# Kernel tuning notes

Measured on AMD Instinct MI355X. Metric: run time of the kernel, lower is better.

Reference implementation:

```python
import jax, jax.numpy as jnp
import numpy as np
from math import factorial, sqrt

# ---- configuration (matches init_kwargs) ----
MUL = 64
N = 32768
IRREPS1 = [(MUL, l) for l in range(3)]   # 64x0e + 64x1o + 64x2e
IRREPS2 = [(1, l) for l in range(3)]     # 1x0e + 1x1o + 1x2e (spherical harmonics)
IRREPS_OUT = [(MUL, l) for l in range(3)]
# (i_in1, i_in2, i_out) -- all parity/triangle-allowed uvw paths with l<=2
PATHS = [(0,0,0),(0,1,1),(0,2,2),(1,0,1),(1,1,0),(1,1,2),(1,2,1),(2,0,2),(2,1,1),(2,2,0),(2,2,2)]

# ---- real Clebsch-Gordan (e3nn convention: real basis, unit Frobenius norm) ----
def _su2_cg(j1, m1, j2, m2, j3, m3):
    if m3 != m1 + m2:
        return 0.0
    f = factorial
    vmin = max(-j1 + j2 + m3, -j1 + m1, 0)
    vmax = min(j2 + j3 + m1, j3 - j1 + j2, j3 + m3)
    C = sqrt((2*j3+1) * f(j3+j1-j2) * f(j3-j1+j2) * f(j1+j2-j3) * f(j3+m3) * f(j3-m3)
             / (f(j1+j2+j3+1) * f(j1-m1) * f(j1+m1) * f(j2-m2) * f(j2+m2)))
    S = 0.0
    for v in range(vmin, vmax + 1):
        S += (-1.0)**(v + j2 + m2) * f(j2+j3+m1-v) * f(j1-m1+v) / (f(v) * f(j3-j1+j2-v) * f(j3+m3-v) * f(v+j1-j2-m3))
    return C * S

def _su2_clebsch_gordan(j1, j2, j3):
    mat = np.zeros((2*j1+1, 2*j2+1, 2*j3+1))
    for m1 in range(-j1, j1+1):
        for m2 in range(-j2, j2+1):
            if abs(m1 + m2) <= j3:
                mat[j1+m1, j2+m2, j3+m1+m2] = _su2_cg(j1, m1, j2, m2, j3, m1+m2)
    return mat

def _change_basis_real_to_complex(l):
    q = np.zeros((2*l+1, 2*l+1), dtype=np.complex128)
    for m in range(-l, 0):
        q[l+m, l+abs(m)] = 1/sqrt(2)
        q[l+m, l-abs(m)] = -1j/sqrt(2)
    q[l, l] = 1
    for m in range(1, l+1):
        q[l+m, l+abs(m)] = (-1)**m / sqrt(2)
        q[l+m, l-abs(m)] = 1j * (-1)**m / sqrt(2)
    return (-1j)**l * q

def clebsch_gordan(l1, l2, l3):
    Q1 = _change_basis_real_to_complex(l1)
    Q2 = _change_basis_real_to_complex(l2)
    Q3 = _change_basis_real_to_complex(l3)
    C = _su2_clebsch_gordan(l1, l2, l3)
    C = np.einsum('ij,kl,mn,ikn->jlm', Q1, Q2, np.conj(Q3.T), C)
    C = np.real(C)
    return C / np.linalg.norm(C)  # unit Frobenius norm (e3nn convention)

# ---- static layout / path weights ----
def _offsets(irreps):
    offs, s = [], 0
    for mul, l in irreps:
        offs.append(s)
        s += mul * (2*l + 1)
    return offs

OFF1, OFF2, OFFO = _offsets(IRREPS1), _offsets(IRREPS2), _offsets(IRREPS_OUT)
# path_normalization='element', irrep_normalization='component'
_norm = {}
for (i1, i2, io) in PATHS:
    _norm[io] = _norm.get(io, 0) + IRREPS1[i1][0] * IRREPS2[i2][0]
PW = [sqrt((2*IRREPS_OUT[io][1] + 1) / _norm[io]) for (_, _, io) in PATHS]


def setup_inputs() -> dict:
    key = jax.random.key(0)
    k1, k2, k3 = jax.random.split(key, 3)
    dim1 = sum(m * (2*l+1) for m, l in IRREPS1)  # 576
    dim2 = sum(m * (2*l+1) for m, l in IRREPS2)  # 9
    nw = sum(IRREPS1[i1][0] * IRREPS2[i2][0] * IRREPS_OUT[io][0] for (i1, i2, io) in PATHS)
    x1 = jax.random.normal(k1, (N, dim1), dtype=jnp.float32)
    x2 = jax.random.normal(k2, (N, dim2), dtype=jnp.float32)
    weights = jax.random.normal(k3, (nw,), dtype=jnp.float32)
    return {"x1": x1, "x2": x2, "weights": weights}


def reference(x1, x2, weights):
    out_acc = [None] * len(IRREPS_OUT)
    wi = 0
    for (i1, i2, io), pw in zip(PATHS, PW):
        m1, l1 = IRREPS1[i1]
        m2, l2 = IRREPS2[i2]
        mo, lo = IRREPS_OUT[io]
        npar = m1 * m2 * mo
        w = weights[wi:wi + npar].reshape(m1, m2, mo)
        wi += npar
        # per-irrep chunks: [N, mul, 2l+1]
        x1c = x1[:, OFF1[i1]:OFF1[i1] + m1 * (2*l1+1)].reshape(-1, m1, 2*l1+1)
        x2c = x2[:, OFF2[i2]:OFF2[i2] + m2 * (2*l2+1)].reshape(-1, m2, 2*l2+1)
        cg = jnp.asarray(pw * clebsch_gordan(l1, l2, lo), dtype=x1.dtype)
        out = jnp.einsum('uvw,ijk,nui,nvj->nwk', w, cg, x1c, x2c)
        out_acc[io] = out if out_acc[io] is None else out_acc[io] + out
    return jnp.concatenate([o.reshape(o.shape[0], -1) for o in out_acc], axis=1)
```

## Files before the change

kernel.cpp:

```cpp
#include <hip/hip_runtime.h>
#include <hip/hip_bf16.h>
#include <cmath>
#include <complex>

#define NDIM1 576
#define NDIM2 9
#define NDIMO 576
#define ROWB 2304
#define TILEB 36864

typedef __attribute__((ext_vector_type(8))) short short8;
typedef __attribute__((ext_vector_type(4))) float f32x4;

struct CGTab { float v[363]; };

union U8 { unsigned short s[8]; short8 v; };

__device__ inline unsigned short f2bf(float x) {
  return __builtin_bit_cast(unsigned short, __float2bfloat16(x));
}

constexpr bool cg_nonzero(int m1, int m2, int m3) {
  int a1 = m1 < 0 ? -m1 : m1, a2 = m2 < 0 ? -m2 : m2, a3 = m3 < 0 ? -m3 : m3;
  int d = a1 > a2 ? a1 - a2 : a2 - a1;
  bool mag = (a3 == a1 + a2) || (a3 == d);
  int neg = (m1 < 0) + (m2 < 0) + (m3 < 0);
  return mag && ((neg & 1) == 0);
}

__global__ __launch_bounds__(256) void prep_w_kernel(const float* __restrict__ W,
                                                     short8* __restrict__ wf) {
  int idx = blockIdx.x * 256 + threadIdx.x;
  if (idx >= 11 * 2 * 4 * 64) return;
  int lane = idx & 63;
  int v = (idx >> 6) & 3;
  int s = (idx >> 8) & 1;
  int p = idx >> 9;
  int g = lane >> 4, r16 = lane & 15;
  const float* wp = W + p * 4096 + (s * 32 + g * 8) * 64 + v * 16 + r16;
  U8 u;
#pragma unroll
  for (int t = 0; t < 8; t++) u.s[t] = f2bf(wp[t * 64]);
  wf[idx] = u.v;
}

typedef __attribute__((address_space(1))) const unsigned int gu32;
typedef __attribute__((address_space(3))) unsigned int lu32;

template <int NI, int OFFB>
__device__ inline void load_lds_chunk(const char* tilebase, int g, int r16,
                                      f32x4 (&raw)[4 * NI]) {
  const char* rowp = tilebase + r16 * ROWB;
  const int rowx = (r16 & 7) << 4;
#pragma unroll
  for (int s = 0; s < 2; s++) {
#pragma unroll
    for (int q = 0; q < 2 * NI; q++) {
      int cb = OFFB + ((s * 32 + g * 8) * NI) * 4 + q * 16;
      raw[s * 2 * NI + q] = *(const f32x4*)(rowp + (cb ^ rowx));
    }
  }
}

template <int NI>
__device__ inline void convert_x1(const f32x4 (&raw)[4 * NI], short8 (&af)[NI][2]) {
#pragma unroll
  for (int s = 0; s < 2; s++) {
#pragma unroll
    for (int i = 0; i < NI; i++) {
      U8 u;
#pragma unroll
      for (int t = 0; t < 8; t++) {
        int idx = t * NI + i;
        u.s[t] = f2bf(raw[s * 2 * NI + (idx >> 2)][idx & 3]);
      }
      af[i][s] = u.v;
    }
  }
}

template <int NI>
__device__ inline void run_path(const short8* __restrict__ wf, int p, int v, int lane,
                                const short8 (&af)[NI][2], f32x4 (&acc)[NI]) {
#pragma unroll
  for (int i = 0; i < NI; i++) acc[i] = (f32x4){0.f, 0.f, 0.f, 0.f};
#pragma unroll
  for (int s = 0; s < 2; s++) {
    short8 b = wf[((p * 2 + s) * 4 + v) * 64 + lane];
#pragma unroll
    for (int i = 0; i < NI; i++)
      acc[i] = __builtin_amdgcn_mfma_f32_16x16x32_bf16(af[i][s], b, acc[i], 0, 0, 0);
  }
}

template <int L1, int L2, int LO, int CGO, int NI>
__device__ inline void epilogue(const float* __restrict__ cg, const f32x4 (&acc)[NI],
                                const float (&x2v)[4][9], float (&outr)[4][9]) {
  constexpr int JO = (L2 == 0) ? 0 : (L2 == 1 ? 1 : 4);
  constexpr int KO = (LO == 0) ? 0 : (LO == 1 ? 1 : 4);
#pragma unroll
  for (int i = 0; i < 2 * L1 + 1; i++) {
#pragma unroll
    for (int j = 0; j < 2 * L2 + 1; j++) {
#pragma unroll
      for (int k = 0; k < 2 * LO + 1; k++) {
        if (!cg_nonzero(i - L1, j - L2, k - LO)) continue;
        float c = cg[CGO + (i * (2 * L2 + 1) + j) * (2 * LO + 1) + k];
#pragma unroll
        for (int r = 0; r < 4; r++)
          outr[r][KO + k] = fmaf(c * x2v[r][JO + j], acc[i][r], outr[r][KO + k]);
      }
    }
  }
}

__global__ __launch_bounds__(256) void TPWithWeights_44925357916441_kernel(
    const float* __restrict__ x1, const float* __restrict__ x2,
    const short8* __restrict__ wf, float* __restrict__ out, CGTab tab) {
  __shared__ float tile[TILEB / 4];

  const int lane = threadIdx.x & 63;
  const int v = threadIdx.x >> 6;
  const int n0 = blockIdx.x << 4;
  const int g = lane >> 4, r16 = lane & 15;
  const float* cg = tab.v;

  const char* x1base = (const char*)(x1 + (size_t)n0 * NDIM1);
#pragma unroll
  for (int ch = 0; ch < 9; ch++) {
    const int c = v * 9 + ch;
    const int P = c * 1024 + lane * 16;
    const int row = P / ROWB;
    const int rem = P - row * ROWB;
    const int sb = rem ^ ((row & 7) << 4);
    const char* src = x1base + row * ROWB + sb;
    __builtin_amdgcn_global_load_lds((gu32*)src, (lu32*)(tile + c * 256), 16, 0, 0);
  }

  f32x4 xv[9];
  {
    const f32x4* p2 = (const f32x4*)(x2 + (size_t)(n0 + g * 4) * NDIM2);
#pragma unroll
    for (int q = 0; q < 9; q++) xv[q] = p2[q];
  }

  float x2v[4][9];
  float outr[4][9];
#pragma unroll
  for (int r = 0; r < 4; r++)
#pragma unroll
    for (int j = 0; j < 9; j++) {
      int idx = r * 9 + j;
      x2v[r][j] = xv[idx >> 2][idx & 3];
      outr[r][j] = 0.f;
    }

  __syncthreads();

  const char* tb = (const char*)tile;

  {
    f32x4 raw[4]; short8 af[1][2]; f32x4 acc[1];
    load_lds_chunk<1, 0>(tb, g, r16, raw);
    convert_x1<1>(raw, af);
    run_path<1>(wf, 0, v, lane, af, acc); epilogue<0, 0, 0, 0, 1>(cg, acc, x2v, outr);
    run_path<1>(wf, 1, v, lane, af, acc); epilogue<0, 1, 1, 1, 1>(cg, acc, x2v, outr);
    run_path<1>(wf, 2, v, lane, af, acc); epilogue<0, 2, 2, 10, 1>(cg, acc, x2v, outr);
  }
  {
    f32x4 raw[12]; short8 af[3][2]; f32x4 acc[3];
    load_lds_chunk<3, 256>(tb, g, r16, raw);
    convert_x1<3>(raw, af);
    run_path<3>(wf, 3, v, lane, af, acc); epilogue<1, 0, 1, 35, 3>(cg, acc, x2v, outr);
    run_path<3>(wf, 4, v, lane, af, acc); epilogue<1, 1, 0, 44, 3>(cg, acc, x2v, outr);
    run_path<3>(wf, 5, v, lane, af, acc); epilogue<1, 1, 2, 53, 3>(cg, acc, x2v, outr);
    run_path<3>(wf, 6, v, lane, af, acc); epilogue<1, 2, 1, 98, 3>(cg, acc, x2v, outr);
  }
  {
    f32x4 raw[20]; short8 af[5][2]; f32x4 acc[5];
    load_lds_chunk<5, 1024>(tb, g, r16, raw);
    convert_x1<5>(raw, af);
    run_path<5>(wf, 7, v, lane, af, acc); epilogue<2, 0, 2, 143, 5>(cg, acc, x2v, outr);
    run_path<5>(wf, 8, v, lane, af, acc); epilogue<2, 1, 1, 168, 5>(cg, acc, x2v, outr);
    run_path<5>(wf, 9, v, lane, af, acc); epilogue<2, 2, 0, 213, 5>(cg, acc, x2v, outr);
    run_path<5>(wf, 10, v, lane, af, acc); epilogue<2, 2, 2, 238, 5>(cg, acc, x2v, outr);
  }

  const int w = v * 16 + r16;
#pragma unroll
  for (int r = 0; r < 4; r++) {
    float* op = out + (size_t)(n0 + g * 4 + r) * NDIMO;
    op[w] = outr[r][0];
#pragma unroll
    for (int k = 0; k < 3; k++) op[64 + w * 3 + k] = outr[r][1 + k];
#pragma unroll
    for (int k = 0; k < 5; k++) op[256 + w * 5 + k] = outr[r][4 + k];
  }
}

static double h_fact(int n) { double r = 1.0; for (int i = 2; i <= n; i++) r *= (double)i; return r; }
static inline int imax3(int a, int b, int c) { int m = a > b ? a : b; return m > c ? m : c; }
static inline int imin3(int a, int b, int c) { int m = a < b ? a : b; return m < c ? m : c; }

static double su2_cg(int j1, int m1, int j2, int m2, int j3, int m3) {
  if (m3 != m1 + m2) return 0.0;
  int vmin = imax3(-j1 + j2 + m3, -j1 + m1, 0);
  int vmax = imin3(j2 + j3 + m1, j3 - j1 + j2, j3 + m3);
  double C = sqrt((2.0 * j3 + 1.0) * h_fact(j3 + j1 - j2) * h_fact(j3 - j1 + j2) *
                  h_fact(j1 + j2 - j3) * h_fact(j3 + m3) * h_fact(j3 - m3) /
                  (h_fact(j1 + j2 + j3 + 1) * h_fact(j1 - m1) * h_fact(j1 + m1) *
                   h_fact(j2 - m2) * h_fact(j2 + m2)));
  double S = 0.0;
  for (int vv = vmin; vv <= vmax; vv++) {
    double sg = ((vv + j2 + m2) & 1) ? -1.0 : 1.0;
    S += sg * h_fact(j2 + j3 + m1 - vv) * h_fact(j1 - m1 + vv) /
         (h_fact(vv) * h_fact(j3 - j1 + j2 - vv) * h_fact(j3 + m3 - vv) * h_fact(vv + j1 - j2 - m3));
  }
  return C * S;
}

static void cb_r2c(int l, std::complex<double> q[5][5]) {
  for (int a = 0; a < 5; a++) for (int b = 0; b < 5; b++) q[a][b] = 0.0;
  const double is2 = 1.0 / sqrt(2.0);
  for (int m = -l; m < 0; m++) {
    q[l + m][l - m] = is2;
    q[l + m][l + m] = std::complex<double>(0.0, -is2);
  }
  q[l][l] = 1.0;
  for (int m = 1; m <= l; m++) {
    double sg = (m & 1) ? -1.0 : 1.0;
    q[l + m][l + m] = sg * is2;
    q[l + m][l - m] = std::complex<double>(0.0, sg * is2);
  }
  std::complex<double> f(1.0, 0.0);
  for (int t = 0; t < l; t++) f *= std::complex<double>(0.0, -1.0);
  for (int a = 0; a < 2 * l + 1; a++) for (int b = 0; b < 2 * l + 1; b++) q[a][b] *= f;
}

static void cg_real(int l1, int l2, int l3, double outm[5][5][5]) {
  std::complex<double> q1[5][5], q2[5][5], q3[5][5];
  cb_r2c(l1, q1); cb_r2c(l2, q2); cb_r2c(l3, q3);
  double nrm = 0.0;
  for (int x = 0; x < 2 * l1 + 1; x++)
    for (int y = 0; y < 2 * l2 + 1; y++)
      for (int z = 0; z < 2 * l3 + 1; z++) {
        std::complex<double> a(0.0, 0.0);
        for (int i = 0; i < 2 * l1 + 1; i++)
          for (int k = 0; k < 2 * l2 + 1; k++)
            for (int n = 0; n < 2 * l3 + 1; n++) {
              double s = su2_cg(l1, i - l1, l2, k - l2, l3, n - l3);
              if (s != 0.0) a += q1[i][x] * q2[k][y] * std::conj(q3[n][z]) * s;
            }
        outm[x][y][z] = a.real();
        nrm += a.real() * a.real();
      }
  nrm = sqrt(nrm);
  for (int x = 0; x < 2 * l1 + 1; x++)
    for (int y = 0; y < 2 * l2 + 1; y++)
      for (int z = 0; z < 2 * l3 + 1; z++) outm[x][y][z] /= nrm;
}

static void build_cg_tables(CGTab& tab) {
  const int PL1[11] = {0, 0, 0, 1, 1, 1, 1, 2, 2, 2, 2};
  const int PL2[11] = {0, 1, 2, 0, 1, 1, 2, 0, 1, 2, 2};
  const int PLO[11] = {0, 1, 2, 1, 0, 2, 1, 2, 1, 0, 2};
  const int CGO[11] = {0, 1, 10, 35, 44, 53, 98, 143, 168, 213, 238};
  const double pw_io[3] = {sqrt(1.0 / 192.0), sqrt(3.0 / 256.0), sqrt(5.0 / 256.0)};
  for (int p = 0; p < 11; p++) {
    int l1 = PL1[p], l2 = PL2[p], lo = PLO[p];
    double c[5][5][5];
    cg_real(l1, l2, lo, c);
    double pw = pw_io[lo];
    for (int i = 0; i < 2 * l1 + 1; i++)
      for (int j = 0; j < 2 * l2 + 1; j++)
        for (int k = 0; k < 2 * lo + 1; k++)
          tab.v[CGO[p] + (i * (2 * l2 + 1) + j) * (2 * lo + 1) + k] = (float)(pw * c[i][j][k]);
  }
}

extern "C" void kernel_launch(void* const* d_in, const int* in_sizes, int n_in,
                              void* d_out, int out_size, void* d_ws, size_t ws_size,
                              hipStream_t stream) {
  const float* x1 = (const float*)d_in[0];
  const float* x2 = (const float*)d_in[1];
  const float* W  = (const float*)d_in[2];
  float* out = (float*)d_out;

  int N = in_sizes[0] / NDIM1;

  CGTab tab;
  build_cg_tables(tab);

  short8* wf = (short8*)d_ws;

  hipLaunchKernelGGL(prep_w_kernel, dim3(22), dim3(256), 0, stream, W, wf);
  hipLaunchKernelGGL(TPWithWeights_44925357916441_kernel, dim3(N / 16), dim3(256), 0, stream,
                     x1, x2, wf, out, tab);
}
```

Baseline: 50.20 us.

## Process four tiles per block with double-buffered LDS prefetch of x1

Each block now loops over four 16-row tiles instead of one. While the current tile is computed, the next tile of x1 is streamed into a second LDS buffer with async global-to-LDS loads, synchronised by a partial vmcnt wait and barriers. The aim is to hide global load latency behind MFMA and epilogue work and to cut per-block setup cost. In exchange, LDS use per block doubles and the grid shrinks fourfold, which may lower occupancy and the latency hiding that came from having many resident blocks.

Result: slower. 54.53 us (+8.6%).

```diff
diff --git a/kernel.cpp b/kernel.cpp
--- a/kernel.cpp
+++ b/kernel.cpp
@@ -8,6 +8,7 @@
 #define NDIMO 576
 #define ROWB 2304
 #define TILEB 36864
+#define TPB 4
 
 typedef __attribute__((ext_vector_type(8))) short short8;
 typedef __attribute__((ext_vector_type(4))) float f32x4;
@@ -117,84 +118,101 @@
 __global__ __launch_bounds__(256) void TPWithWeights_44925357916441_kernel(
     const float* __restrict__ x1, const float* __restrict__ x2,
     const short8* __restrict__ wf, float* __restrict__ out, CGTab tab) {
-  __shared__ float tile[TILEB / 4];
+  __shared__ float tile[2][TILEB / 4];
 
   const int lane = threadIdx.x & 63;
   const int v = threadIdx.x >> 6;
-  const int n0 = blockIdx.x << 4;
   const int g = lane >> 4, r16 = lane & 15;
+  const int t0 = blockIdx.x * TPB;
   const float* cg = tab.v;
 
-  const char* x1base = (const char*)(x1 + (size_t)n0 * NDIM1);
-#pragma unroll
-  for (int ch = 0; ch < 9; ch++) {
-    const int c = v * 9 + ch;
-    const int P = c * 1024 + lane * 16;
-    const int row = P / ROWB;
-    const int rem = P - row * ROWB;
-    const int sb = rem ^ ((row & 7) << 4);
-    const char* src = x1base + row * ROWB + sb;
-    __builtin_amdgcn_global_load_lds((gu32*)src, (lu32*)(tile + c * 256), 16, 0, 0);
-  }
-
-  f32x4 xv[9];
-  {
-    const f32x4* p2 = (const f32x4*)(x2 + (size_t)(n0 + g * 4) * NDIM2);
-#pragma unroll
-    for (int q = 0; q < 9; q++) xv[q] = p2[q];
-  }
-
-  float x2v[4][9];
-  float outr[4][9];
-#pragma unroll
-  for (int r = 0; r < 4; r++)
-#pragma unroll
-    for (int j = 0; j < 9; j++) {
-      int idx = r * 9 + j;
-      x2v[r][j] = xv[idx >> 2][idx & 3];
-      outr[r][j] = 0.f;
-    }
-
-  __syncthreads();
-
-  const char* tb = (const char*)tile;
-
-  {
-    f32x4 raw[4]; short8 af[1][2]; f32x4 acc[1];
-    load_lds_chunk<1, 0>(tb, g, r16, raw);
-    convert_x1<1>(raw, af);
-    run_path<1>(wf, 0, v, lane, af, acc); epilogue<0, 0, 0, 0, 1>(cg, acc, x2v, outr);
-    run_path<1>(wf, 1, v, lane, af, acc); epilogue<0, 1, 1, 1, 1>(cg, acc, x2v, outr);
-    run_path<1>(wf, 2, v, lane, af, acc); epilogue<0, 2, 2, 10, 1>(cg, acc, x2v, outr);
-  }
-  {
-    f32x4 raw[12]; short8 af[3][2]; f32x4 acc[3];
-    load_lds_chunk<3, 256>(tb, g, r16, raw);
-    convert_x1<3>(raw, af);
-    run_path<3>(wf, 3, v, lane, af, acc); epilogue<1, 0, 1, 35, 3>(cg, acc, x2v, outr);
-    run_path<3>(wf, 4, v, lane, af, acc); epilogue<1, 1, 0, 44, 3>(cg, acc, x2v, outr);
-    run_path<3>(wf, 5, v, lane, af, acc); epilogue<1, 1, 2, 53, 3>(cg, acc, x2v, outr);
-    run_path<3>(wf, 6, v, lane, af, acc); epilogue<1, 2, 1, 98, 3>(cg, acc, x2v, outr);
-  }
-  {
-    f32x4 raw[20]; short8 af[5][2]; f32x4 acc[5];
-    load_lds_chunk<5, 1024>(tb, g, r16, raw);
-    convert_x1<5>(raw, af);
-    run_path<5>(wf, 7, v, lane, af, acc); epilogue<2, 0, 2, 143, 5>(cg, acc, x2v, outr);
-    run_path<5>(wf, 8, v, lane, af, acc); epilogue<2, 1, 1, 168, 5>(cg, acc, x2v, outr);
-    run_path<5>(wf, 9, v, lane, af, acc); epilogue<2, 2, 0, 213, 5>(cg, acc, x2v, outr);
-    run_path<5>(wf, 10, v, lane, af, acc); epilogue<2, 2, 2, 238, 5>(cg, acc, x2v, outr);
-  }
-
-  const int w = v * 16 + r16;
-#pragma unroll
-  for (int r = 0; r < 4; r++) {
-    float* op = out + (size_t)(n0 + g * 4 + r) * NDIMO;
-    op[w] = outr[r][0];
-#pragma unroll
-    for (int k = 0; k < 3; k++) op[64 + w * 3 + k] = outr[r][1 + k];
-#pragma unroll
-    for (int k = 0; k < 5; k++) op[256 + w * 5 + k] = outr[r][4 + k];
+  auto stage = [&](int nt, int b) {
+    const char* x1base = (const char*)(x1 + (size_t)(nt << 4) * NDIM1);
+#pragma unroll
+    for (int ch = 0; ch < 9; ch++) {
+      const int c = v * 9 + ch;
+      const int P = c * 1024 + lane * 16;
+      const int row = P / ROWB;
+      const int rem = P - row * ROWB;
+      const int sb = rem ^ ((row & 7) << 4);
+      __builtin_amdgcn_global_load_lds((gu32*)(x1base + row * ROWB + sb),
+                                       (lu32*)(&tile[b][0] + c * 256), 16, 0, 0);
+    }
+  };
+
+  stage(t0, 0);
+
+  for (int t = 0; t < TPB; t++) {
+    const int n0 = (t0 + t) << 4;
+    const int cur = t & 1;
+
+    if (t + 1 < TPB) stage(t0 + t + 1, cur ^ 1);
+
+    asm volatile("s_waitcnt vmcnt(9)" ::: "memory");
+    __builtin_amdgcn_sched_barrier(0);
+    __builtin_amdgcn_s_barrier();
+    __builtin_amdgcn_sched_barrier(0);
+
+    f32x4 xv[9];
+    {
+      const f32x4* p2 = (const f32x4*)(x2 + (size_t)(n0 + g * 4) * NDIM2);
+#pragma unroll
+      for (int q = 0; q < 9; q++) xv[q] = p2[q];
+    }
+    float x2v[4][9];
+    float outr[4][9];
+#pragma unroll
+    for (int r = 0; r < 4; r++)
+#pragma unroll
+      for (int j = 0; j < 9; j++) {
+        int idx = r * 9 + j;
+        x2v[r][j] = xv[idx >> 2][idx & 3];
+        outr[r][j] = 0.f;
+      }
+
+    const char* tb = (const char*)&tile[cur][0];
+
+    {
+      f32x4 raw[4]; short8 af[1][2]; f32x4 acc[1];
+      load_lds_chunk<1, 0>(tb, g, r16, raw);
+      convert_x1<1>(raw, af);
+      run_path<1>(wf, 0, v, lane, af, acc); epilogue<0, 0, 0, 0, 1>(cg, acc, x2v, outr);
+      run_path<1>(wf, 1, v, lane, af, acc); epilogue<0, 1, 1, 1, 1>(cg, acc, x2v, outr);
+      run_path<1>(wf, 2, v, lane, af, acc); epilogue<0, 2, 2, 10, 1>(cg, acc, x2v, outr);
+    }
+    {
+      f32x4 raw[12]; short8 af[3][2]; f32x4 acc[3];
+      load_lds_chunk<3, 256>(tb, g, r16, raw);
+      convert_x1<3>(raw, af);
+      run_path<3>(wf, 3, v, lane, af, acc); epilogue<1, 0, 1, 35, 3>(cg, acc, x2v, outr);
+      run_path<3>(wf, 4, v, lane, af, acc); epilogue<1, 1, 0, 44, 3>(cg, acc, x2v, outr);
+      run_path<3>(wf, 5, v, lane, af, acc); epilogue<1, 1, 2, 53, 3>(cg, acc, x2v, outr);
+      run_path<3>(wf, 6, v, lane, af, acc); epilogue<1, 2, 1, 98, 3>(cg, acc, x2v, outr);
+    }
+    {
+      f32x4 raw[20]; short8 af[5][2]; f32x4 acc[5];
+      load_lds_chunk<5, 1024>(tb, g, r16, raw);
+      convert_x1<5>(raw, af);
+      run_path<5>(wf, 7, v, lane, af, acc); epilogue<2, 0, 2, 143, 5>(cg, acc, x2v, outr);
+      run_path<5>(wf, 8, v, lane, af, acc); epilogue<2, 1, 1, 168, 5>(cg, acc, x2v, outr);
+      run_path<5>(wf, 9, v, lane, af, acc); epilogue<2, 2, 0, 213, 5>(cg, acc, x2v, outr);
+      run_path<5>(wf, 10, v, lane, af, acc); epilogue<2, 2, 2, 238, 5>(cg, acc, x2v, outr);
+    }
+
+    const int w = v * 16 + r16;
+#pragma unroll
+    for (int r = 0; r < 4; r++) {
+      float* op = out + (size_t)(n0 + g * 4 + r) * NDIMO;
+      op[w] = outr[r][0];
+#pragma unroll
+      for (int k = 0; k < 3; k++) op[64 + w * 3 + k] = outr[r][1 + k];
+#pragma unroll
+      for (int k = 0; k < 5; k++) op[256 + w * 5 + k] = outr[r][4 + k];
+    }
+
+    __builtin_amdgcn_sched_barrier(0);
+    __builtin_amdgcn_s_barrier();
+    __builtin_amdgcn_sched_barrier(0);
   }
 }
 
@@ -294,6 +312,6 @@
   short8* wf = (short8*)d_ws;
 
   hipLaunchKernelGGL(prep_w_kernel, dim3(22), dim3(256), 0, stream, W, wf);
-  hipLaunchKernelGGL(TPWithWeights_44925357916441_kernel, dim3(N / 16), dim3(256), 0, stream,
-                     x1, x2, wf, out, tab);
-}
+  hipLaunchKernelGGL(TPWithWeights_44925357916441_kernel, dim3(N / (16 * TPB)), dim3(256), 0,
+                     stream, x1, x2, wf, out, tab);
+}
```
